# Optimization experiments

Measured on AMD Instinct MI355X. Metric: run time of the kernel, lower is better.

Reference implementation:

```python
import jax, jax.numpy as jnp
import numpy as np

C = 1.0          # Poincare ball curvature
TEMP = 0.1       # softmax temperature
EPS = 1e-15
TANH_CLIP = 1.0 - 1e-5


def setup_inputs() -> dict:
    key = jax.random.key(0)
    ks = jax.random.split(key, 9)
    B, Din, H, D, P = 2048, 1024, 4096, 128, 1000
    inp = {
        "x": jax.random.normal(ks[0], (B, Din), dtype=jnp.float32),
        "W1": jax.random.normal(ks[1], (Din, H), dtype=jnp.float32) / np.sqrt(Din),
        "b1": jnp.zeros((H,), dtype=jnp.float32),
        "W2": jax.random.normal(ks[2], (H, H), dtype=jnp.float32) / np.sqrt(H),
        "b2": jnp.zeros((H,), dtype=jnp.float32),
        "W3": jax.random.normal(ks[3], (H, D), dtype=jnp.float32) / np.sqrt(H),
        "b3": jnp.zeros((D,), dtype=jnp.float32),
        # prototypes: points inside the unit ball (norm ~ 0.2)
        "prototypes": jax.random.normal(ks[4], (P, D), dtype=jnp.float32) * 0.02,
    }
    return inp


def _expmap0(u):
    sqc = np.sqrt(C)
    n = jnp.maximum(jnp.linalg.norm(u, axis=-1, keepdims=True), EPS)
    return jnp.tanh(sqc * n) * u / (sqc * n)


def _logmap0(y):
    sqc = np.sqrt(C)
    n = jnp.maximum(jnp.linalg.norm(y, axis=-1, keepdims=True), EPS)
    arg = jnp.clip(sqc * n, 0.0, TANH_CLIP)
    return jnp.arctanh(arg) * y / (sqc * n)


def _pairwise_dist(proto, xh):
    # dist(x=proto[P,D], y=xh[B,D]) = (2/sqrt(c)) * artanh(sqrt(c)*||(-x) (+) y||)
    # Mobius add norm computed from Gram products only (no [B,P,D] intermediate).
    # a = -proto, b = xh
    a2 = jnp.sum(proto * proto, axis=-1)          # [P]  ||a||^2
    b2 = jnp.sum(xh * xh, axis=-1)                # [B]  ||b||^2
    ab = -jnp.einsum('bd,pd->bp', xh, proto)      # [B,P] <a,b>
    a2_ = a2[None, :]
    b2_ = b2[:, None]
    alpha = 1.0 + 2.0 * C * ab + C * b2_
    beta = 1.0 - C * a2_
    gamma = 1.0 + 2.0 * C * ab + (C * C) * a2_ * b2_
    m2 = (alpha * alpha * a2_ + 2.0 * alpha * beta * ab + beta * beta * b2_) / (gamma * gamma)
    mnorm = jnp.sqrt(jnp.maximum(m2, 0.0))
    sqc = np.sqrt(C)
    arg = jnp.clip(sqc * mnorm, 0.0, TANH_CLIP)
    return (2.0 / sqc) * jnp.arctanh(arg)         # [B,P]


def reference(x, W1, b1, W2, b2, W3, b3, prototypes):
    h = jax.nn.gelu(x @ W1 + b1, approximate=False)
    h = jax.nn.gelu(h @ W2 + b2, approximate=False)
    u = h @ W3 + b3                               # [B,D]
    x_hyp = _expmap0(u)
    dists = _pairwise_dist(prototypes, x_hyp)     # [B,P]
    logits = -dists / TEMP
    pred = jnp.argmax(logits, axis=1)             # [B]
    pred_protos = jax.lax.stop_gradient(prototypes[pred])  # detach, as in torch
    feedback = _logmap0(pred_protos)              # [B,D]
    return logits, feedback
```

## Files before the change

kernel.cpp:

```cpp
#include <hip/hip_runtime.h>
#include <math.h>

#define B_SZ 2048
#define DIN  1024
#define H_SZ 4096
#define D_SZ 128
#define P_SZ 1000
#define PPAD 1024

typedef __attribute__((ext_vector_type(8))) short bf16x8;
typedef __attribute__((ext_vector_type(4))) float f32x4;

__device__ __forceinline__ float gelu_exact(float v) {
    return 0.5f * v * (1.0f + erff(v * 0.70710678118654752f));
}

__device__ __forceinline__ short f2bf(float f) {
    unsigned u = __float_as_uint(f);
    u = (u + 0x7fffu + ((u >> 16) & 1u)) >> 16;
    return (short)u;
}

__device__ __forceinline__ void gload_lds16(const void* g, void* l) {
    __builtin_amdgcn_global_load_lds(
        (__attribute__((address_space(1))) void*)(uintptr_t)g,
        (__attribute__((address_space(3))) void*)(uintptr_t)l,
        16, 0, 0);
}

__device__ __forceinline__ void trans_tile(
    const float* __restrict__ W, short* __restrict__ WT, int K, int N,
    int bx, int by, int tid, float (*t)[65])
{
    const int n0 = bx * 64, k0 = by * 64;
    #pragma unroll
    for (int i = 0; i < 4; ++i) {
        const int idx = i * 256 + tid;
        const int r  = idx >> 4;
        const int c4 = (idx & 15) * 4;
        const float4 v = *reinterpret_cast<const float4*>(&W[(size_t)(k0 + r) * N + n0 + c4]);
        t[r][c4 + 0] = v.x; t[r][c4 + 1] = v.y; t[r][c4 + 2] = v.z; t[r][c4 + 3] = v.w;
    }
    __syncthreads();
    #pragma unroll
    for (int i = 0; i < 2; ++i) {
        const int idx = i * 256 + tid;
        const int n  = idx >> 3;
        const int kc = (idx & 7) * 8;
        bf16x8 o;
        #pragma unroll
        for (int q = 0; q < 8; ++q) o[q] = f2bf(t[kc + q][n]);
        *reinterpret_cast<bf16x8*>(&WT[(size_t)(n0 + n) * K + k0 + kc]) = o;
    }
}

__global__ __launch_bounds__(256) void prep_kernel(
    const float* __restrict__ x,     short* __restrict__ xb,
    const float* __restrict__ W1,    short* __restrict__ w1t,
    const float* __restrict__ W2,    short* __restrict__ w2t,
    const float* __restrict__ W3,    short* __restrict__ w3t,
    const float* __restrict__ proto, short* __restrict__ protob,
    float* __restrict__ a2gp)
{
    __shared__ float t[64][65];
    __shared__ float part[4];
    const int b = blockIdx.x;
    const int tid = threadIdx.x;

    if (b < 2048) {
        const int i = b * 1024 + tid * 4;
        const float4 v = *reinterpret_cast<const float4*>(&x[i]);
        short4 o;
        o.x = f2bf(v.x); o.y = f2bf(v.y); o.z = f2bf(v.z); o.w = f2bf(v.w);
        *reinterpret_cast<short4*>(&xb[i]) = o;
    } else if (b < 3072) {
        const int tt = b - 2048;
        trans_tile(W1, w1t, DIN, H_SZ, tt & 63, tt >> 6, tid, t);
    } else if (b < 7168) {
        const int tt = b - 3072;
        trans_tile(W2, w2t, H_SZ, H_SZ, tt & 63, tt >> 6, tid, t);
    } else if (b < 7296) {
        const int tt = b - 7168;
        trans_tile(W3, w3t, H_SZ, D_SZ, tt & 1, tt >> 1, tid, t);
    } else {
        const int h = tid >> 7;
        const int d = tid & 127;
        const int p = (b - 7296) * 2 + h;
        const float y = (p < P_SZ) ? proto[(size_t)p * D_SZ + d] : 0.f;
        protob[(size_t)p * D_SZ + d] = f2bf(y);
        float s = y * y;
        #pragma unroll
        for (int off = 32; off; off >>= 1) s += __shfl_down(s, off);
        if ((tid & 63) == 0) part[tid >> 6] = s;
        __syncthreads();
        if (d == 0) a2gp[p] = part[h * 2] + part[h * 2 + 1];
    }
}

template<int EPI>
__global__ __launch_bounds__(512) void gemm_big(
    const short* __restrict__ A, const short* __restrict__ BT,
    const float* __restrict__ bias, void* __restrict__ Cout,
    int M, int N, int K)
{
    extern __shared__ __align__(16) char smem[];

    const int tid  = threadIdx.x;
    const int lane = tid & 63;
    const int wid  = tid >> 6;
    const int row0 = blockIdx.y * 256;
    const int col0 = blockIdx.x * 128;
    const int wm = (wid >> 1) * 64;
    const int wn = (wid & 1) * 64;
    const int lr = lane & 15, kq = lane >> 4;

    const int kpb    = K / gridDim.z;
    const int kstart = blockIdx.z * kpb;
    const int NT = kpb >> 6;

    f32x4 acc[4][4];
    #pragma unroll
    for (int i = 0; i < 4; ++i)
        #pragma unroll
        for (int j = 0; j < 4; ++j) acc[i][j] = (f32x4){0.f, 0.f, 0.f, 0.f};

    const int srow = lane >> 3;
    const int kch  = (lane & 7) ^ srow;
    const short* Ag = A  + (size_t)(row0 + wid * 32 + srow) * K + kstart + kch * 8;
    const short* Bg = BT + (size_t)(col0 + wid * 16 + srow) * K + kstart + kch * 8;

    auto stage = [&](int t) {
        const int buf = t % 3;
        char* sA = smem + buf * 49152;
        char* sB = sA + 32768;
        const int k0 = t << 6;
        #pragma unroll
        for (int ii = 0; ii < 4; ++ii)
            gload_lds16(Ag + (size_t)ii * 8 * K + k0, sA + (wid * 4 + ii) * 1024);
        #pragma unroll
        for (int ii = 0; ii < 2; ++ii)
            gload_lds16(Bg + (size_t)ii * 8 * K + k0, sB + (wid * 2 + ii) * 1024);
    };

    stage(0);
    stage(1);
    asm volatile("s_waitcnt vmcnt(6)" ::: "memory");
    __builtin_amdgcn_s_barrier();
    asm volatile("" ::: "memory");

    for (int t = 0; t < NT; ++t) {
        const bool more = (t + 2) < NT;
        if (more) stage(t + 2);

        const char* sA = smem + (t % 3) * 49152;
        const char* sB = sA + 32768;

        #pragma unroll
        for (int ks = 0; ks < 2; ++ks) {
            bf16x8 af[4], bfv[4];
            #pragma unroll
            for (int i = 0; i < 4; ++i) {
                const int row = wm + i * 16 + lr;
                af[i] = *reinterpret_cast<const bf16x8*>(
                    sA + row * 128 + (((ks * 4 + kq) ^ (lr & 7)) * 16));
            }
            #pragma unroll
            for (int j = 0; j < 4; ++j) {
                const int row = wn + j * 16 + lr;
                bfv[j] = *reinterpret_cast<const bf16x8*>(
                    sB + row * 128 + (((ks * 4 + kq) ^ (lr & 7)) * 16));
            }
            __builtin_amdgcn_s_setprio(1);
            #pragma unroll
            for (int i = 0; i < 4; ++i)
                #pragma unroll
                for (int j = 0; j < 4; ++j)
                    acc[i][j] = __builtin_amdgcn_mfma_f32_16x16x32_bf16(
                        af[i], bfv[j], acc[i][j], 0, 0, 0);
            __builtin_amdgcn_s_setprio(0);
        }

        asm volatile("" ::: "memory");
        if (more) asm volatile("s_waitcnt vmcnt(6) lgkmcnt(0)" ::: "memory");
        else      asm volatile("s_waitcnt vmcnt(0) lgkmcnt(0)" ::: "memory");
        __builtin_amdgcn_s_barrier();
        asm volatile("" ::: "memory");
    }

    #pragma unroll
    for (int j = 0; j < 4; ++j) {
        const int col = col0 + wn + j * 16 + lr;
        const float bv = (EPI == 0) ? bias[col] : 0.f;
        #pragma unroll
        for (int i = 0; i < 4; ++i) {
            #pragma unroll
            for (int q = 0; q < 4; ++q) {
                const int row = row0 + wm + i * 16 + kq * 4 + q;
                if (EPI == 0) {
                    float v = gelu_exact(acc[i][j][q] + bv);
                    ((short*)Cout)[(size_t)row * N + col] = f2bf(v);
                } else {
                    ((float*)Cout)[((size_t)blockIdx.z * M + row) * N + col] = acc[i][j][q];
                }
            }
        }
    }
}

__global__ __launch_bounds__(256) void gemm_m128(
    const short* __restrict__ A, const short* __restrict__ BT,
    const float* __restrict__ bias, short* __restrict__ Cout,
    int M, int N, int K)
{
    __shared__ __align__(16) short sA[3][4][128][8];
    __shared__ __align__(16) short sB[3][4][128][8];

    const int tid  = threadIdx.x;
    const int lane = tid & 63;
    const int wid  = tid >> 6;
    const int row0 = blockIdx.y * 128;
    const int col0 = blockIdx.x * 128;
    const int wm = (wid >> 1) * 64;
    const int wn = (wid & 1) * 64;
    const int lr = lane & 15, kq = lane >> 4;

    const int NT = K >> 5;

    f32x4 acc[4][4];
    #pragma unroll
    for (int i = 0; i < 4; ++i)
        #pragma unroll
        for (int j = 0; j < 4; ++j) acc[i][j] = (f32x4){0.f, 0.f, 0.f, 0.f};

    const short* Ag = A  + (size_t)(row0 + lane) * K + wid * 8;
    const short* Bg = BT + (size_t)(col0 + lane) * K + wid * 8;

    auto stage = [&](int t) {
        const int buf = t % 3;
        const int k0 = t << 5;
        #pragma unroll
        for (int ii = 0; ii < 2; ++ii) {
            gload_lds16(Ag + (size_t)(ii * 64) * K + k0, &sA[buf][wid][ii * 64][0]);
            gload_lds16(Bg + (size_t)(ii * 64) * K + k0, &sB[buf][wid][ii * 64][0]);
        }
    };

    stage(0);
    stage(1);
    asm volatile("s_waitcnt vmcnt(4)" ::: "memory");
    __builtin_amdgcn_s_barrier();
    asm volatile("" ::: "memory");

    for (int t = 0; t < NT; ++t) {
        const bool more = (t + 2) < NT;
        if (more) stage(t + 2);
        const int buf = t % 3;

        bf16x8 af[4], bfv[4];
        #pragma unroll
        for (int i = 0; i < 4; ++i)
            af[i] = *reinterpret_cast<const bf16x8*>(&sA[buf][kq][wm + i * 16 + lr][0]);
        #pragma unroll
        for (int j = 0; j < 4; ++j)
            bfv[j] = *reinterpret_cast<const bf16x8*>(&sB[buf][kq][wn + j * 16 + lr][0]);

        __builtin_amdgcn_s_setprio(1);
        #pragma unroll
        for (int i = 0; i < 4; ++i)
            #pragma unroll
            for (int j = 0; j < 4; ++j)
                acc[i][j] = __builtin_amdgcn_mfma_f32_16x16x32_bf16(
                    af[i], bfv[j], acc[i][j], 0, 0, 0);
        __builtin_amdgcn_s_setprio(0);

        asm volatile("" ::: "memory");
        if (more) asm volatile("s_waitcnt vmcnt(4) lgkmcnt(0)" ::: "memory");
        else      asm volatile("s_waitcnt vmcnt(0) lgkmcnt(0)" ::: "memory");
        __builtin_amdgcn_s_barrier();
        asm volatile("" ::: "memory");
    }

    #pragma unroll
    for (int j = 0; j < 4; ++j) {
        const int col = col0 + wn + j * 16 + lr;
        const float bv = bias[col];
        #pragma unroll
        for (int i = 0; i < 4; ++i) {
            #pragma unroll
            for (int q = 0; q < 4; ++q) {
                const int row = row0 + wm + i * 16 + kq * 4 + q;
                float v = gelu_exact(acc[i][j][q] + bv);
                Cout[(size_t)row * N + col] = f2bf(v);
            }
        }
    }
}

__global__ __launch_bounds__(128) void expmap_kernel(
    const float* __restrict__ up, const float* __restrict__ b3,
    short* __restrict__ xhb, float* __restrict__ rowb2)
{
    const int b = blockIdx.x;
    const int d = threadIdx.x;
    float u = b3[d];
    #pragma unroll
    for (int z = 0; z < 16; ++z)
        u += up[((size_t)z * B_SZ + b) * D_SZ + d];

    float s = u * u;
    #pragma unroll
    for (int off = 32; off; off >>= 1) s += __shfl_down(s, off);
    __shared__ float part[2];
    if ((d & 63) == 0) part[d >> 6] = s;
    __syncthreads();
    const float n2 = part[0] + part[1];

    const float n = fmaxf(sqrtf(n2), 1e-15f);
    const float t = tanhf(n);
    xhb[(size_t)b * D_SZ + d] = f2bf(u * (t / n));
    if (d == 0) rowb2[b] = t * t;
}

__global__ __launch_bounds__(256) void dist_mfma(
    const short* __restrict__ xhb, const short* __restrict__ protob,
    const float* __restrict__ rowb2, const float* __restrict__ a2gp,
    float* __restrict__ logits)
{
    __shared__ __align__(16) char xs[128 * 256];
    __shared__ __align__(16) char ps[64 * 256];

    const int tid  = threadIdx.x;
    const int lane = tid & 63, wid = tid >> 6;
    const int pt = blockIdx.x * 64;
    const int bt = blockIdx.y * 128;
    const int wm = (wid >> 1) * 64;
    const int wn = (wid & 1) * 32;
    const int lr = lane & 15, kq = lane >> 4;

    const int rl = lane >> 4, c = lane & 15;
    #pragma unroll
    for (int i = 0; i < 8; ++i) {
        const int row = wid * 32 + i * 4 + rl;
        const int lc  = (c & 8) | ((c & 7) ^ (row & 7));
        gload_lds16(xhb + (size_t)(bt + row) * D_SZ + lc * 8,
                    xs + (wid * 8 + i) * 1024);
    }
    #pragma unroll
    for (int i = 0; i < 4; ++i) {
        const int row = wid * 16 + i * 4 + rl;
        const int lc  = (c & 8) | ((c & 7) ^ (row & 7));
        gload_lds16(protob + (size_t)(pt + row) * D_SZ + lc * 8,
                    ps + (wid * 4 + i) * 1024);
    }
    __syncthreads();

    f32x4 acc[4][2];
    #pragma unroll
    for (int i = 0; i < 4; ++i)
        #pragma unroll
        for (int j = 0; j < 2; ++j) acc[i][j] = (f32x4){0.f, 0.f, 0.f, 0.f};

    #pragma unroll
    for (int ks = 0; ks < 4; ++ks) {
        const int kslot = ks * 4 + kq;
        bf16x8 af[4], bfv[2];
        #pragma unroll
        for (int i = 0; i < 4; ++i) {
            const int row = wm + i * 16 + lr;
            const int ph = (kslot & 8) | ((kslot & 7) ^ (row & 7));
            af[i] = *reinterpret_cast<const bf16x8*>(xs + row * 256 + ph * 16);
        }
        #pragma unroll
        for (int j = 0; j < 2; ++j) {
            const int row = wn + j * 16 + lr;
            const int ph = (kslot & 8) | ((kslot & 7) ^ (row & 7));
            bfv[j] = *reinterpret_cast<const bf16x8*>(ps + row * 256 + ph * 16);
        }
        #pragma unroll
        for (int i = 0; i < 4; ++i)
            #pragma unroll
            for (int j = 0; j < 2; ++j)
                acc[i][j] = __builtin_amdgcn_mfma_f32_16x16x32_bf16(
                    af[i], bfv[j], acc[i][j], 0, 0, 0);
    }

    #pragma unroll
    for (int j = 0; j < 2; ++j) {
        const int p = pt + wn + j * 16 + lr;
        if (p < P_SZ) {
            const float a2 = a2gp[p];
            #pragma unroll
            for (int i = 0; i < 4; ++i) {
                #pragma unroll
                for (int q = 0; q < 4; ++q) {
                    const int b = bt + wm + i * 16 + kq * 4 + q;
                    const float b2 = rowb2[b];
                    const float ab = -acc[i][j][q];
                    const float alpha = 1.f + 2.f * ab + b2;
                    const float beta  = 1.f - a2;
                    const float gamma = 1.f + 2.f * ab + a2 * b2;
                    const float num = alpha * alpha * a2 + 2.f * alpha * beta * ab + beta * beta * b2;
                    const float m2 = num / (gamma * gamma);
                    const float mn = sqrtf(fmaxf(m2, 0.f));
                    const float arg = fminf(mn, 0.99999f);
                    const float dist = logf((1.f + arg) / (1.f - arg));
                    logits[(size_t)b * P_SZ + p] = -10.f * dist;
                }
            }
        }
    }
}

__global__ __launch_bounds__(256) void head_kernel(
    const float* __restrict__ logits, const float* __restrict__ proto,
    float* __restrict__ fb)
{
    const int b = blockIdx.x;
    const int tid = threadIdx.x;

    float best = -INFINITY; int bi = 0;
    for (int p = tid; p < P_SZ; p += 256) {
        const float v = logits[(size_t)b * P_SZ + p];
        if (v > best) { best = v; bi = p; }
    }
    __shared__ float bv[256];
    __shared__ int   bidx[256];
    bv[tid] = best; bidx[tid] = bi;
    __syncthreads();
    for (int s = 128; s; s >>= 1) {
        if (tid < s) {
            const float ov = bv[tid + s]; const int oi = bidx[tid + s];
            if (ov > bv[tid] || (ov == bv[tid] && oi < bidx[tid])) { bv[tid] = ov; bidx[tid] = oi; }
        }
        __syncthreads();
    }
    const int pred = bidx[0];
    __syncthreads();

    float y = 0.f;
    if (tid < 128) y = proto[(size_t)pred * D_SZ + tid];
    bv[tid] = y * y;
    __syncthreads();
    for (int s = 128; s; s >>= 1) {
        if (tid < s) bv[tid] += bv[tid + s];
        __syncthreads();
    }
    const float n2 = bv[0];
    if (tid < 128) {
        const float n = fmaxf(sqrtf(n2), 1e-15f);
        const float arg = fminf(n, 0.99999f);
        const float at = 0.5f * logf((1.f + arg) / (1.f - arg));
        fb[(size_t)b * D_SZ + tid] = at * (y / n);
    }
}

extern "C" void kernel_launch(void* const* d_in, const int* in_sizes, int n_in,
                              void* d_out, int out_size, void* d_ws, size_t ws_size,
                              hipStream_t stream)
{
    const float* x     = (const float*)d_in[0];
    const float* W1    = (const float*)d_in[1];
    const float* b1    = (const float*)d_in[2];
    const float* W2    = (const float*)d_in[3];
    const float* b2v   = (const float*)d_in[4];
    const float* W3    = (const float*)d_in[5];
    const float* b3    = (const float*)d_in[6];
    const float* proto = (const float*)d_in[7];

    float* logits = (float*)d_out;
    float* fb     = logits + (size_t)B_SZ * P_SZ;

    short* xb     = (short*)d_ws;
    short* w1t    = xb    + (size_t)B_SZ * DIN;
    short* w2t    = w1t   + (size_t)H_SZ * DIN;
    short* w3t    = w2t   + (size_t)H_SZ * H_SZ;
    short* h1     = w3t   + (size_t)D_SZ * H_SZ;
    short* h2     = h1    + (size_t)B_SZ * H_SZ;
    short* xhb    = h2    + (size_t)B_SZ * H_SZ;
    short* protob = xhb   + (size_t)B_SZ * D_SZ;
    float* rowb2  = (float*)(protob + (size_t)PPAD * D_SZ);
    float* a2gp   = rowb2 + B_SZ;
    float* up     = (float*)h1;

    static_cast<void>(hipFuncSetAttribute(
        reinterpret_cast<const void*>(&gemm_big<0>),
        hipFuncAttributeMaxDynamicSharedMemorySize, 3 * 49152));
    static_cast<void>(hipFuncSetAttribute(
        reinterpret_cast<const void*>(&gemm_big<1>),
        hipFuncAttributeMaxDynamicSharedMemorySize, 3 * 49152));

    prep_kernel<<<7808, 256, 0, stream>>>(x, xb, W1, w1t, W2, w2t, W3, w3t,
                                          proto, protob, a2gp);

    gemm_m128<<<dim3(H_SZ / 128, B_SZ / 128), 256, 0, stream>>>(
        xb, w1t, b1, h1, B_SZ, H_SZ, DIN);
    gemm_big<0><<<dim3(H_SZ / 128, B_SZ / 256), 512, 3 * 49152, stream>>>(
        h1, w2t, b2v, h2, B_SZ, H_SZ, H_SZ);
    gemm_big<1><<<dim3(1, B_SZ / 256, 16), 512, 3 * 49152, stream>>>(
        h2, w3t, nullptr, up, B_SZ, D_SZ, H_SZ);

    expmap_kernel<<<B_SZ, 128, 0, stream>>>(up, b3, xhb, rowb2);
    dist_mfma<<<dim3(PPAD / 64, B_SZ / 128), 256, 0, stream>>>(
        xhb, protob, rowb2, a2gp, logits);
    head_kernel<<<B_SZ, 256, 0, stream>>>(logits, proto, fb);
}
```

Baseline: 280.3 us.

## Use 256x256 split-K GEMM with swizzled LDS for layer 2, add GELU combine

Replaces the layer-2 GEMM with a new 256x256-tile kernel using 8 waves, XOR-swizzled LDS, a double buffer and phased loads interleaved with MFMA. K is split in two, giving 256 blocks, and each half writes bf16 partials. A separate elementwise kernel then sums the partials, adds the bias and applies GELU. Layer 1 now uses gemm_big<0> instead of gemm_m128. Storing the partials in bf16 adds rounding error and extra memory traffic in exchange for better tile reuse and occupancy.

```diff
diff --git a/kernel.cpp b/kernel.cpp
--- a/kernel.cpp
+++ b/kernel.cpp
@@ -19,6 +19,10 @@
     unsigned u = __float_as_uint(f);
     u = (u + 0x7fffu + ((u >> 16) & 1u)) >> 16;
     return (short)u;
+}
+__device__ __forceinline__ float bf2f(short s) {
+    unsigned u = ((unsigned)(unsigned short)s) << 16;
+    return __uint_as_float(u);
 }
 
 __device__ __forceinline__ void gload_lds16(const void* g, void* l) {
@@ -207,93 +211,167 @@
     }
 }
 
-__global__ __launch_bounds__(256) void gemm_m128(
+__global__ __launch_bounds__(512) void gemm_ph8(
     const short* __restrict__ A, const short* __restrict__ BT,
-    const float* __restrict__ bias, short* __restrict__ Cout,
+    short* __restrict__ P0, short* __restrict__ P1,
     int M, int N, int K)
 {
-    __shared__ __align__(16) short sA[3][4][128][8];
-    __shared__ __align__(16) short sB[3][4][128][8];
+    extern __shared__ __align__(16) char smem[];
 
     const int tid  = threadIdx.x;
     const int lane = tid & 63;
     const int wid  = tid >> 6;
-    const int row0 = blockIdx.y * 128;
-    const int col0 = blockIdx.x * 128;
-    const int wm = (wid >> 1) * 64;
-    const int wn = (wid & 1) * 64;
+    const int row0 = blockIdx.y * 256;
+    const int col0 = blockIdx.x * 256;
+    const int wm = wid >> 2;
+    const int wn = wid & 3;
     const int lr = lane & 15, kq = lane >> 4;
 
-    const int NT = K >> 5;
-
-    f32x4 acc[4][4];
-    #pragma unroll
-    for (int i = 0; i < 4; ++i)
+    const int kstart = blockIdx.z * (K >> 1);
+    const int NT = (K >> 1) >> 6;
+
+    f32x4 acc[8][4];
+    #pragma unroll
+    for (int i = 0; i < 8; ++i)
         #pragma unroll
         for (int j = 0; j < 4; ++j) acc[i][j] = (f32x4){0.f, 0.f, 0.f, 0.f};
 
-    const short* Ag = A  + (size_t)(row0 + lane) * K + wid * 8;
-    const short* Bg = BT + (size_t)(col0 + lane) * K + wid * 8;
-
-    auto stage = [&](int t) {
-        const int buf = t % 3;
-        const int k0 = t << 5;
-        #pragma unroll
-        for (int ii = 0; ii < 2; ++ii) {
-            gload_lds16(Ag + (size_t)(ii * 64) * K + k0, &sA[buf][wid][ii * 64][0]);
-            gload_lds16(Bg + (size_t)(ii * 64) * K + k0, &sB[buf][wid][ii * 64][0]);
-        }
+    const int srow8 = lane >> 3;
+    const int kchs  = (lane & 7) ^ srow8;
+    const short* Asrc = A  + (size_t)(row0 + wid * 16 + srow8) * K + kstart + kchs * 8;
+    const short* Bsrc = BT + (size_t)(col0 + wid * 16 + srow8) * K + kstart + kchs * 8;
+
+    auto stA = [&](int t, int h) {
+        char* d = smem + (t & 1) * 32768 + h * 16384 + wid * 2048;
+        const short* s = Asrc + (size_t)(h * 128) * K + (t << 6);
+        gload_lds16(s, d);
+        gload_lds16(s + (size_t)8 * K, d + 1024);
     };
-
-    stage(0);
-    stage(1);
-    asm volatile("s_waitcnt vmcnt(4)" ::: "memory");
+    auto stB = [&](int t, int h) {
+        char* d = smem + 65536 + (t & 1) * 32768 + h * 16384 + wid * 2048;
+        const short* s = Bsrc + (size_t)(h * 128) * K + (t << 6);
+        gload_lds16(s, d);
+        gload_lds16(s + (size_t)8 * K, d + 1024);
+    };
+
+    stA(0, 0); stA(0, 1); stB(0, 0); stB(0, 1);
+    asm volatile("s_waitcnt vmcnt(0)" ::: "memory");
     __builtin_amdgcn_s_barrier();
     asm volatile("" ::: "memory");
 
     for (int t = 0; t < NT; ++t) {
-        const bool more = (t + 2) < NT;
-        if (more) stage(t + 2);
-        const int buf = t % 3;
-
-        bf16x8 af[4], bfv[4];
-        #pragma unroll
-        for (int i = 0; i < 4; ++i)
-            af[i] = *reinterpret_cast<const bf16x8*>(&sA[buf][kq][wm + i * 16 + lr][0]);
+        const bool more = (t + 1) < NT;
+        const char* sAb = smem + (t & 1) * 32768 + wm * 16384;
+        const char* sBb = smem + 65536 + (t & 1) * 32768 + (wn >> 1) * 16384;
+        const int bro = (wn & 1) * 64;
+        bf16x8 a0[4], a1[4], bv[4];
+
+        #pragma unroll
+        for (int i = 0; i < 4; ++i)
+            a0[i] = *reinterpret_cast<const bf16x8*>(
+                sAb + (i * 16 + lr) * 128 + ((kq ^ (lr & 7)) * 16));
         #pragma unroll
         for (int j = 0; j < 4; ++j)
-            bfv[j] = *reinterpret_cast<const bf16x8*>(&sB[buf][kq][wn + j * 16 + lr][0]);
-
+            bv[j] = *reinterpret_cast<const bf16x8*>(
+                sBb + (bro + j * 16 + lr) * 128 + ((kq ^ (lr & 7)) * 16));
+        if (more) { stA(t + 1, 0); stA(t + 1, 1); }
+        __builtin_amdgcn_s_barrier();
+        asm volatile("s_waitcnt lgkmcnt(0)" ::: "memory");
+        __builtin_amdgcn_sched_barrier(0);
         __builtin_amdgcn_s_setprio(1);
         #pragma unroll
         for (int i = 0; i < 4; ++i)
             #pragma unroll
             for (int j = 0; j < 4; ++j)
-                acc[i][j] = __builtin_amdgcn_mfma_f32_16x16x32_bf16(
-                    af[i], bfv[j], acc[i][j], 0, 0, 0);
+                acc[i][j] = __builtin_amdgcn_mfma_f32_16x16x32_bf16(a0[i], bv[j], acc[i][j], 0, 0, 0);
         __builtin_amdgcn_s_setprio(0);
-
+        __builtin_amdgcn_s_barrier();
+
+        #pragma unroll
+        for (int i = 0; i < 4; ++i)
+            a1[i] = *reinterpret_cast<const bf16x8*>(
+                sAb + ((i + 4) * 16 + lr) * 128 + ((kq ^ (lr & 7)) * 16));
+        if (more) { stB(t + 1, 0); stB(t + 1, 1); }
+        __builtin_amdgcn_s_barrier();
+        asm volatile("s_waitcnt lgkmcnt(0)" ::: "memory");
+        __builtin_amdgcn_sched_barrier(0);
+        __builtin_amdgcn_s_setprio(1);
+        #pragma unroll
+        for (int i = 0; i < 4; ++i)
+            #pragma unroll
+            for (int j = 0; j < 4; ++j)
+                acc[i + 4][j] = __builtin_amdgcn_mfma_f32_16x16x32_bf16(a1[i], bv[j], acc[i + 4][j], 0, 0, 0);
+        __builtin_amdgcn_s_setprio(0);
+        __builtin_amdgcn_s_barrier();
+
+        #pragma unroll
+        for (int i = 0; i < 4; ++i)
+            a0[i] = *reinterpret_cast<const bf16x8*>(
+                sAb + (i * 16 + lr) * 128 + (((4 + kq) ^ (lr & 7)) * 16));
+        #pragma unroll
+        for (int j = 0; j < 4; ++j)
+            bv[j] = *reinterpret_cast<const bf16x8*>(
+                sBb + (bro + j * 16 + lr) * 128 + (((4 + kq) ^ (lr & 7)) * 16));
+        __builtin_amdgcn_s_barrier();
+        asm volatile("s_waitcnt lgkmcnt(0)" ::: "memory");
+        __builtin_amdgcn_sched_barrier(0);
+        __builtin_amdgcn_s_setprio(1);
+        #pragma unroll
+        for (int i = 0; i < 4; ++i)
+            #pragma unroll
+            for (int j = 0; j < 4; ++j)
+                acc[i][j] = __builtin_amdgcn_mfma_f32_16x16x32_bf16(a0[i], bv[j], acc[i][j], 0, 0, 0);
+        __builtin_amdgcn_s_setprio(0);
+        __builtin_amdgcn_s_barrier();
+
+        #pragma unroll
+        for (int i = 0; i < 4; ++i)
+            a1[i] = *reinterpret_cast<const bf16x8*>(
+                sAb + ((i + 4) * 16 + lr) * 128 + (((4 + kq) ^ (lr & 7)) * 16));
+        __builtin_amdgcn_s_barrier();
+        asm volatile("s_waitcnt lgkmcnt(0)" ::: "memory");
+        __builtin_amdgcn_sched_barrier(0);
+        __builtin_amdgcn_s_setprio(1);
+        #pragma unroll
+        for (int i = 0; i < 4; ++i)
+            #pragma unroll
+            for (int j = 0; j < 4; ++j)
+                acc[i + 4][j] = __builtin_amdgcn_mfma_f32_16x16x32_bf16(a1[i], bv[j], acc[i + 4][j], 0, 0, 0);
+        __builtin_amdgcn_s_setprio(0);
+        if (more) asm volatile("s_waitcnt vmcnt(0)" ::: "memory");
+        __builtin_amdgcn_s_barrier();
         asm volatile("" ::: "memory");
-        if (more) asm volatile("s_waitcnt vmcnt(4) lgkmcnt(0)" ::: "memory");
-        else      asm volatile("s_waitcnt vmcnt(0) lgkmcnt(0)" ::: "memory");
-        __builtin_amdgcn_s_barrier();
-        asm volatile("" ::: "memory");
-    }
-
+    }
+
+    short* P = blockIdx.z ? P1 : P0;
     #pragma unroll
     for (int j = 0; j < 4; ++j) {
-        const int col = col0 + wn + j * 16 + lr;
-        const float bv = bias[col];
-        #pragma unroll
-        for (int i = 0; i < 4; ++i) {
+        const int col = col0 + wn * 64 + j * 16 + lr;
+        #pragma unroll
+        for (int i = 0; i < 8; ++i) {
             #pragma unroll
             for (int q = 0; q < 4; ++q) {
-                const int row = row0 + wm + i * 16 + kq * 4 + q;
-                float v = gelu_exact(acc[i][j][q] + bv);
-                Cout[(size_t)row * N + col] = f2bf(v);
+                const int row = row0 + wm * 128 + i * 16 + kq * 4 + q;
+                P[(size_t)row * N + col] = f2bf(acc[i][j][q]);
             }
         }
     }
+}
+
+__global__ __launch_bounds__(256) void gelu_combine(
+    const short* __restrict__ p0, const short* __restrict__ p1,
+    const float* __restrict__ bias, short* __restrict__ h2)
+{
+    const int i = (blockIdx.x * 256 + threadIdx.x) * 4;
+    const short4 v0 = *reinterpret_cast<const short4*>(&p0[i]);
+    const short4 v1 = *reinterpret_cast<const short4*>(&p1[i]);
+    const int col = i & (H_SZ - 1);
+    short4 o;
+    o.x = f2bf(gelu_exact(bf2f(v0.x) + bf2f(v1.x) + bias[col + 0]));
+    o.y = f2bf(gelu_exact(bf2f(v0.y) + bf2f(v1.y) + bias[col + 1]));
+    o.z = f2bf(gelu_exact(bf2f(v0.z) + bf2f(v1.z) + bias[col + 2]));
+    o.w = f2bf(gelu_exact(bf2f(v0.w) + bf2f(v1.w) + bias[col + 3]));
+    *reinterpret_cast<short4*>(&h2[i]) = o;
 }
 
 __global__ __launch_bounds__(128) void expmap_kernel(
@@ -480,6 +558,7 @@
     short* protob = xhb   + (size_t)B_SZ * D_SZ;
     float* rowb2  = (float*)(protob + (size_t)PPAD * D_SZ);
     float* a2gp   = rowb2 + B_SZ;
+    short* gp1    = (short*)(a2gp + PPAD);
     float* up     = (float*)h1;
 
     static_cast<void>(hipFuncSetAttribute(
@@ -488,14 +567,18 @@
     static_cast<void>(hipFuncSetAttribute(
         reinterpret_cast<const void*>(&gemm_big<1>),
         hipFuncAttributeMaxDynamicSharedMemorySize, 3 * 49152));
+    static_cast<void>(hipFuncSetAttribute(
+        reinterpret_cast<const void*>(&gemm_ph8),
+        hipFuncAttributeMaxDynamicSharedMemorySize, 131072));
 
     prep_kernel<<<7808, 256, 0, stream>>>(x, xb, W1, w1t, W2, w2t, W3, w3t,
                                           proto, protob, a2gp);
 
-    gemm_m128<<<dim3(H_SZ / 128, B_SZ / 128), 256, 0, stream>>>(
+    gemm_big<0><<<dim3(H_SZ / 128, B_SZ / 256), 512, 3 * 49152, stream>>>(
         xb, w1t, b1, h1, B_SZ, H_SZ, DIN);
-    gemm_big<0><<<dim3(H_SZ / 128, B_SZ / 256), 512, 3 * 49152, stream>>>(
-        h1, w2t, b2v, h2, B_SZ, H_SZ, H_SZ);
+    gemm_ph8<<<dim3(H_SZ / 256, B_SZ / 256, 2), 512, 131072, stream>>>(
+        h1, w2t, h2, gp1, B_SZ, H_SZ, H_SZ);
+    gelu_combine<<<(B_SZ * H_SZ) / 1024, 256, 0, stream>>>(h2, gp1, b2v, h2);
     gemm_big<1><<<dim3(1, B_SZ / 256, 16), 512, 3 * 49152, stream>>>(
         h2, w3t, nullptr, up, B_SZ, D_SZ, H_SZ);
 
```

After: 276.3 us. Within noise of the previous version (-1.4%).
